# Kernel optimization log

Hardware: AMD Instinct MI355X
Metric: run time of the kernel (lower is better)

Reference implementation:

```python
import math
import jax, jax.numpy as jnp
import numpy as np

B, L, H, D = 1, 2048, 16, 64
M = 24            # nb_features
WINDOW = 128      # local_context / window_size
SCALE = 0.125     # softmax_scale = 1/sqrt(D)
MASK_VAL = -10000.0
EPS = 1e-4        # SBPerformerFeatures eps


def setup_inputs() -> dict:
    key = jax.random.key(0)
    k1, k2 = jax.random.split(key)
    qkv = jax.random.normal(k1, (B, L, 3, H, D), dtype=jnp.float32)
    proj = jax.random.normal(k2, (M, D), dtype=jnp.float32)  # Performer random features
    return {"qkv": qkv, "proj": proj}


def _performer_features(x, proj, is_query):
    # Softmax-kernel random features with separate log scale (scatterbrain SBPerformerFeatures).
    # exp(t*q.k) ~= exp(q_log + k_log) * <q_prime, k_prime>
    dn = math.sqrt(SCALE)
    xs = x * dn                                            # (b,h,l,d)
    x_dash = jnp.einsum('bhld,md->bhlm', xs, proj)         # (b,h,l,m)
    x_norm = 0.5 * jnp.sum(xs * xs, axis=-1, keepdims=True)
    half_log_m = 0.5 * math.log(M)
    if is_query:
        stab = jax.lax.stop_gradient(jnp.max(x_dash, axis=-1, keepdims=True))
        prime = jnp.exp(x_dash - stab) + EPS               # per-row stabilized
        log_scale = stab - x_norm - half_log_m             # (b,h,l,1)
    else:
        stab = jax.lax.stop_gradient(jnp.max(x_dash, axis=(-1, -2), keepdims=True))
        prime = jnp.exp(x_dash - x_norm - stab) + EPS      # norm folded in (needed for cumsum)
        log_scale = stab - half_log_m                      # (b,h,1,1)
    return prime, log_scale


def _band_mask(n):
    idx = jnp.arange(n)
    diff = idx[:, None] - idx[None, :]                     # i - j
    return jnp.where((diff >= 0) & (diff <= WINDOW), 0.0, MASK_VAL)  # (L,L)


def _forward(qkv, proj):
    q, k, v = qkv[:, :, 0], qkv[:, :, 1], qkv[:, :, 2]     # (b,l,h,d)
    q = jnp.transpose(q, (0, 2, 1, 3))                     # (b,h,l,d)
    k = jnp.transpose(k, (0, 2, 1, 3))
    v = jnp.transpose(v, (0, 2, 1, 3))

    # --- GlobalPerformer path ---
    q_prime, q_log = _performer_features(q, proj, True)    # (b,h,l,m), (b,h,l,1)
    k_prime, k_log = _performer_features(k, proj, False)   # (b,h,l,m), (b,h,1,1)
    global_scale = q_log + k_log                           # (b,h,l,1)

    k_cum = jnp.cumsum(k_prime, axis=2)
    global_out_cumsum = jnp.einsum('bhlm,bhlm->bhl', q_prime, k_cum)
    # causal_dot_product: out_i = q'_i . sum_{j<=i} k'_j v_j^T
    kv = jnp.cumsum(k_prime[..., :, None] * v[..., None, :], axis=2)   # (b,h,l,m,d)
    global_out = jnp.einsum('bhlm,bhlmd->bhld', q_prime, kv)

    mask = _band_mask(L)
    p_scores = jnp.einsum('bhme,bhne->bhmn', q_prime, k_prime) * SCALE
    global_qk = jnp.maximum(p_scores + mask[None, None], 0.0)  # masked_fill(<=0, 0)

    # --- Local exact softmax path ---
    scores = jnp.einsum('bhme,bhne->bhmn', q, k) * SCALE
    local_qk = scores + mask[None, None]
    qk_lse = jax.scipy.special.logsumexp(local_qk, axis=-1, keepdims=True)  # (b,h,l,1)

    gqk_sum = jnp.sum(global_qk, axis=-1, keepdims=True)
    global_log_norm = jnp.log(jnp.maximum(global_out_cumsum[..., None] - gqk_sum, 1e-24)) + global_scale
    log_norm = jnp.logaddexp(qk_lse, global_log_norm)      # (b,h,l,1)
    global_prime_scale = jnp.exp(global_scale - log_norm)  # (b,h,l,1)

    local_score = jax.nn.softmax(local_qk - log_norm, axis=-1) - global_qk * global_prime_scale
    out = jnp.einsum('bhmn,bhnd->bhmd', local_score, v) + global_out * global_prime_scale
    return jnp.transpose(out, (0, 2, 1, 3))                # (b,l,h,d)


def reference(qkv, proj):
    return _forward(qkv, proj)
```

## Files before the change

kernel.cpp:

```cpp
#include <hip/hip_runtime.h>
#include <hip/hip_bf16.h>

#define L_SEQ 2048
#define NH 16
#define DH 64
#define NCH 32
#define SCALE_F 0.125f
#define EPS_F 1e-4f
#define DN_F 0.35355339059327373f
#define HLM_F 1.5890269151739727f

typedef __attribute__((ext_vector_type(8))) short short8v;
typedef __attribute__((ext_vector_type(4))) float f32x4;

__device__ __forceinline__ unsigned short f2bf(float x) {
  unsigned u = __float_as_uint(x);
  u += 0x7FFFu + ((u >> 16) & 1u);
  return (unsigned short)(u >> 16);
}
__device__ __forceinline__ unsigned pk2(float a, float b) {
  return (unsigned)f2bf(a) | ((unsigned)f2bf(b) << 16);
}
__device__ __forceinline__ float stab_from_pmax(const float* __restrict__ pmax, int h, int t) {
  float v = pmax[h * 32 + (t & 31)];
  v = fmaxf(v, __shfl_xor(v, 1));  v = fmaxf(v, __shfl_xor(v, 2));
  v = fmaxf(v, __shfl_xor(v, 4));  v = fmaxf(v, __shfl_xor(v, 8));
  v = fmaxf(v, __shfl_xor(v, 16));
  return v;
}

__global__ __launch_bounds__(256) void k1_feat(
    const float* __restrict__ qkv, const float* __restrict__ proj,
    float* __restrict__ kdash, float* __restrict__ knorm,
    float* __restrict__ qdash, float* __restrict__ qnorm,
    float* __restrict__ pmax, unsigned* __restrict__ kbw, unsigned* __restrict__ qbw)
{
  __shared__ __attribute__((aligned(16))) float sP[24][68];
  __shared__ __attribute__((aligned(16))) float sX[64][68];
  __shared__ float sRed[256];
  const int c = blockIdx.x, h = blockIdx.y, qk = blockIdx.z, t = threadIdx.x;
  const int slot = qk ? 0 : 1;
  for (int i = t; i < 24 * 64; i += 256) sP[i >> 6][i & 63] = proj[i];
  for (int i = t; i < 1024; i += 256) {
    int rr = i >> 4, d4 = (i & 15) * 4;
    int l = c * 64 + rr;
    *(float4*)&sX[rr][d4] = *(const float4*)(qkv + (((size_t)l * 3 + slot) * NH + h) * DH + d4);
  }
  __syncthreads();
  unsigned* dstw = qk ? qbw : kbw;
  for (int w = t; w < 2048; w += 256) {
    int rr = w >> 5, wo = w & 31;
    int l = c * 64 + rr;
    float2 xv = *(const float2*)&sX[rr][2 * wo];
    dstw[((size_t)h * L_SEQ + l) * 32 + (wo ^ ((rr & 7) << 2))] = pk2(xv.x, xv.y);
  }
  const int r = t >> 2, mg = t & 3;
  float acc[6] = {0.f, 0.f, 0.f, 0.f, 0.f, 0.f};
  float sq = 0.f;
  for (int d4 = 0; d4 < 16; ++d4) {
    float4 xv = *(const float4*)&sX[r][d4 * 4];
    sq += xv.x * xv.x; sq += xv.y * xv.y; sq += xv.z * xv.z; sq += xv.w * xv.w;
#pragma unroll
    for (int i = 0; i < 6; ++i) {
      float4 pv = *(const float4*)&sP[mg * 6 + i][d4 * 4];
      acc[i] += xv.x * pv.x; acc[i] += xv.y * pv.y;
      acc[i] += xv.z * pv.z; acc[i] += xv.w * pv.w;
    }
  }
  int l = c * 64 + r;
  float* dsh = qk ? qdash : kdash;
  float lmax = -1e30f;
#pragma unroll
  for (int i = 0; i < 6; ++i) {
    float v = acc[i] * DN_F;
    dsh[((size_t)h * L_SEQ + l) * 24 + mg * 6 + i] = v;
    lmax = fmaxf(lmax, v);
  }
  if (mg == 0) (qk ? qnorm : knorm)[h * L_SEQ + l] = 0.5f * SCALE_F * sq;
  if (qk == 0) {
    sRed[t] = lmax;
    __syncthreads();
#pragma unroll
    for (int s = 128; s > 0; s >>= 1) {
      if (t < s) sRed[t] = fmaxf(sRed[t], sRed[t + s]);
      __syncthreads();
    }
    if (t == 0) pmax[h * 32 + c] = sRed[0];
  }
}

__global__ __launch_bounds__(256) void k3_kprime(
    const float* __restrict__ qkv, const float* __restrict__ kdash,
    const float* __restrict__ knorm, const float* __restrict__ pmax,
    unsigned* __restrict__ kpw, float* __restrict__ kpfx, float* __restrict__ kvs,
    unsigned* __restrict__ vtw)
{
  __shared__ float sKp[64][25];
  __shared__ __attribute__((aligned(16))) float sV[64][68];
  const int c = blockIdx.x, h = blockIdx.y, t = threadIdx.x;
  const float stab = stab_from_pmax(pmax, h, t);
  for (int i = t; i < 1024; i += 256) {
    int rr = i >> 4, d4 = (i & 15) * 4;
    int l = c * 64 + rr;
    *(float4*)&sV[rr][d4] = *(const float4*)(qkv + (((size_t)l * 3 + 2) * NH + h) * DH + d4);
  }
  for (int i = t; i < 1536; i += 256) {
    int r = i / 24, m = i % 24;
    int l = c * 64 + r;
    sKp[r][m] = __expf(kdash[((size_t)h * L_SEQ + l) * 24 + m] - knorm[h * L_SEQ + l] - stab) + EPS_F;
  }
  __syncthreads();
  for (int w = t; w < 1024; w += 256) {
    int r = w >> 4, wo = w & 15;
    int l = c * 64 + r;
    float a = (wo < 12) ? sKp[r][2 * wo] : 0.f;
    float bb = (wo < 12) ? sKp[r][2 * wo + 1] : 0.f;
    kpw[((size_t)h * L_SEQ + l) * 16 + (wo ^ ((r & 3) << 2))] = pk2(a, bb);
  }
  for (int w = t; w < 2048; w += 256) {
    int d = w >> 5, jp = w & 31;
    vtw[((size_t)h * NCH + c) * 2048 + d * 32 + (jp ^ ((d & 7) << 2))] = pk2(sV[2 * jp][d], sV[2 * jp + 1][d]);
  }
  if (t < 192) {
    const int m = t % 24, dO = (t / 24) * 8;
    float a0x = 0.f, a0y = 0.f, a0z = 0.f, a0w = 0.f;
    float a1x = 0.f, a1y = 0.f, a1z = 0.f, a1w = 0.f;
    for (int r2 = 0; r2 < 64; ++r2) {
      float kp = sKp[r2][m];
      float4 v0 = *(const float4*)&sV[r2][dO];
      float4 v1 = *(const float4*)&sV[r2][dO + 4];
      a0x += kp * v0.x; a0y += kp * v0.y; a0z += kp * v0.z; a0w += kp * v0.w;
      a1x += kp * v1.x; a1y += kp * v1.y; a1z += kp * v1.z; a1w += kp * v1.w;
    }
    float* dst = kvs + ((size_t)h * NCH + c) * 1536 + m * 64 + dO;
    float4 o0 = {a0x, a0y, a0z, a0w};
    float4 o1 = {a1x, a1y, a1z, a1w};
    *(float4*)dst = o0;
    *(float4*)(dst + 4) = o1;
  }
  if (t < 24) {
    float run = 0.f;
    for (int r2 = 0; r2 < 64; ++r2) {
      run += sKp[r2][t];
      kpfx[((size_t)h * L_SEQ + c * 64 + r2) * 24 + t] = run;
    }
  }
}

__global__ __launch_bounds__(256, 2) void k6_attn(
    const unsigned* __restrict__ kpw, const float* __restrict__ kpfx,
    const float* __restrict__ kvs, const unsigned* __restrict__ vtw,
    const float* __restrict__ qdash, const float* __restrict__ qnorm,
    const float* __restrict__ pmax, const unsigned* __restrict__ kbw,
    const unsigned* __restrict__ qbw, float* __restrict__ out)
{
  __shared__ __attribute__((aligned(16))) char lds[56160];
  char* sKW = lds;
  char* sKp = lds + 24576;
  char* sQV = lds + 36864;
  char* sQp = lds + 45056;
  float* sSum = (float*)(lds + 49152);
  float* sGps = sSum + 64;
  float* sRin = sGps + 64;
  float* sKcx = (float*)(lds + 49920);
  float* sPfx = (float*)(lds + 50016);

  const int b = blockIdx.x, h = blockIdx.y, t = threadIdx.x;
  const int wv = t >> 6, lane = t & 63, g = lane >> 4, ln = lane & 15;
  const int keybase = b * 64 - 128;
  const int jmin = (b >= 2) ? 0 : (128 - 64 * b);
  const int rA = wv * 16 + ln;

  for (int w = t; w < 1536; w += 256) {
    int r = w >> 3, q4 = w & 7;
    int l = keybase + r; l = l < 0 ? 0 : l;
    *(uint4*)(sKW + r * 128 + q4 * 16) = *(const uint4*)(kbw + ((size_t)h * L_SEQ + l) * 32 + q4 * 4);
  }
  for (int w = t; w < 512; w += 256) {
    int r = w >> 3, q4 = w & 7;
    int l = b * 64 + r;
    *(uint4*)(sQV + r * 128 + q4 * 16) = *(const uint4*)(qbw + ((size_t)h * L_SEQ + l) * 32 + q4 * 4);
  }
  for (int w = t; w < 768; w += 256) {
    int r = w >> 2, q4 = w & 3;
    int l = keybase + r; l = l < 0 ? 0 : l;
    *(uint4*)(sKp + r * 64 + q4 * 16) = *(const uint4*)(kpw + ((size_t)h * L_SEQ + l) * 16 + q4 * 4);
  }
  const float stab = stab_from_pmax(pmax, h, t);
  {
    float accp[6] = {0.f, 0.f, 0.f, 0.f, 0.f, 0.f};
    const float* srcb = kvs + (size_t)h * NCH * 1536 + t;
    int bp = 0;
    for (; bp + 4 <= b; bp += 4) {
      float v0[6], v1[6], v2[6], v3[6];
#pragma unroll
      for (int j = 0; j < 6; ++j) v0[j] = srcb[(size_t)(bp + 0) * 1536 + j * 256];
#pragma unroll
      for (int j = 0; j < 6; ++j) v1[j] = srcb[(size_t)(bp + 1) * 1536 + j * 256];
#pragma unroll
      for (int j = 0; j < 6; ++j) v2[j] = srcb[(size_t)(bp + 2) * 1536 + j * 256];
#pragma unroll
      for (int j = 0; j < 6; ++j) v3[j] = srcb[(size_t)(bp + 3) * 1536 + j * 256];
#pragma unroll
      for (int j = 0; j < 6; ++j) {
        accp[j] += v0[j]; accp[j] += v1[j]; accp[j] += v2[j]; accp[j] += v3[j];
      }
    }
    for (; bp < b; ++bp) {
#pragma unroll
      for (int j = 0; j < 6; ++j) accp[j] += srcb[(size_t)bp * 1536 + j * 256];
    }
#pragma unroll
    for (int j = 0; j < 6; ++j) sPfx[t + j * 256] = accp[j];
  }
  if (t < 24) {
    float runk = 0.f;
    for (int bp = 0; bp < b; ++bp)
      runk += kpfx[((size_t)h * L_SEQ + bp * 64 + 63) * 24 + t];
    sKcx[t] = runk;
  }
  float qlog = 0.f;
  float qpv[24];
  if (t < 64) {
    int r = t, l = b * 64 + r;
    const float* qdp = qdash + ((size_t)h * L_SEQ + l) * 24;
    float qd[24], mx = -1e30f;
#pragma unroll
    for (int m = 0; m < 24; ++m) { qd[m] = qdp[m]; mx = fmaxf(mx, qd[m]); }
#pragma unroll
    for (int m = 0; m < 24; ++m) qpv[m] = __expf(qd[m] - mx) + EPS_F;
    qlog = mx - qnorm[h * L_SEQ + l] - HLM_F;
#pragma unroll
    for (int wo = 0; wo < 16; ++wo) {
      float a = (wo < 12) ? qpv[2 * wo] : 0.f;
      float bb = (wo < 12) ? qpv[2 * wo + 1] : 0.f;
      *(unsigned*)(sQp + (r * 64 + (((wo * 4)) ^ ((r & 3) << 4)))) = pk2(a, bb);
    }
  }
  __syncthreads();

  float eF[12][4];
  float rs[4] = {0.f, 0.f, 0.f, 0.f};
  short8v aS0 = *(const short8v*)(sQV + (rA * 128 + ((g * 16) ^ ((rA & 7) << 4))));
  short8v aS1 = *(const short8v*)(sQV + (rA * 128 + ((64 + g * 16) ^ ((rA & 7) << 4))));
#pragma unroll
  for (int nt = 0; nt < 12; ++nt) {
    int rB = nt * 16 + ln;
    short8v b0 = *(const short8v*)(sKW + (rB * 128 + ((g * 16) ^ ((rB & 7) << 4))));
    short8v b1 = *(const short8v*)(sKW + (rB * 128 + ((64 + g * 16) ^ ((rB & 7) << 4))));
    f32x4 acc = {0.f, 0.f, 0.f, 0.f};
    acc = __builtin_amdgcn_mfma_f32_16x16x32_bf16(aS0, b0, acc, 0, 0, 0);
    acc = __builtin_amdgcn_mfma_f32_16x16x32_bf16(aS1, b1, acc, 0, 0, 0);
    int j = nt * 16 + ln;
#pragma unroll
    for (int reg = 0; reg < 4; ++reg) {
      int rl = wv * 16 + g * 4 + reg;
      float e = 0.f;
      if (j >= rl && j <= rl + 128 && j >= jmin) e = __expf(SCALE_F * acc[reg]);
      eF[nt][reg] = e;
      rs[reg] += e;
    }
  }
#pragma unroll
  for (int reg = 0; reg < 4; ++reg) {
    float v = rs[reg];
    v += __shfl_xor(v, 1); v += __shfl_xor(v, 2);
    v += __shfl_xor(v, 4); v += __shfl_xor(v, 8);
    if (ln == 0) sSum[wv * 16 + g * 4 + reg] = v;
  }

  float pF[12][4];
  short8v aP = *(const short8v*)(sQp + (rA * 64 + ((g * 16) ^ ((rA & 3) << 4))));
#pragma unroll
  for (int nt = 0; nt < 12; ++nt) {
    int rB = nt * 16 + ln;
    short8v bp = *(const short8v*)(sKp + (rB * 64 + ((g * 16) ^ ((rB & 3) << 4))));
    f32x4 acc = {0.f, 0.f, 0.f, 0.f};
    acc = __builtin_amdgcn_mfma_f32_16x16x32_bf16(aP, bp, acc, 0, 0, 0);
#pragma unroll
    for (int reg = 0; reg < 4; ++reg) pF[nt][reg] = acc[reg];
  }
  __syncthreads();

  if (t < 64) {
    int r = t, l = b * 64 + r;
    const float* kfc = kpfx + ((size_t)h * L_SEQ + l) * 24;
    int b1i = (b >= 1) ? b - 1 : 0;
    int b2i = (b >= 2) ? b - 2 : 0;
    int rm1 = (r >= 1) ? r - 1 : 0;
    const float* T1p = kpfx + ((size_t)h * L_SEQ + b1i * 64 + 63) * 24;
    const float* T2p = kpfx + ((size_t)h * L_SEQ + b2i * 64 + 63) * 24;
    const float* S2p = kpfx + ((size_t)h * L_SEQ + b2i * 64 + rm1) * 24;
    float f1 = (b >= 1) ? 1.f : 0.f;
    float f2 = (b >= 2) ? 1.f : 0.f;
    float fr = (b >= 2 && r >= 1) ? 1.f : 0.f;
    float psc = 0.f, kcs = 0.f, bnd = 0.f;
#pragma unroll
    for (int m = 0; m < 24; ++m) {
      float qp = qpv[m];
      float kc = kfc[m];
      psc += qp * kc;
      kcs += qp * sKcx[m];
      bnd += qp * (kc + f1 * T1p[m] + f2 * T2p[m] - fr * S2p[m]);
    }
    float goc = kcs + psc;
    float gqk = SCALE_F * bnd;
    float se = sSum[r];
    float lse = __logf(se);
    float gscale = qlog + stab - HLM_F;
    float gln = __logf(fmaxf(goc - gqk, 1e-24f)) + gscale;
    float mx2 = fmaxf(lse, gln), mn2 = fminf(lse, gln);
    float lognorm = mx2 + log1pf(__expf(mn2 - mx2));
    sGps[r] = __expf(gscale - lognorm);
    sRin[r] = 1.f / se;
  }
  __syncthreads();

  float gpr[4], rin[4];
#pragma unroll
  for (int reg = 0; reg < 4; ++reg) {
    int rl = wv * 16 + g * 4 + reg;
    gpr[reg] = sGps[rl];
    rin[reg] = sRin[rl];
  }
#pragma unroll
  for (int nt = 0; nt < 12; ++nt) {
    int j = nt * 16 + ln;
#pragma unroll
    for (int reg = 0; reg < 4; ++reg) {
      int rl = wv * 16 + g * 4 + reg;
      bool causal = (j >= 128) && (j <= 128 + rl);
      bool bprev = (j >= rl) && (j < 128) && (j >= jmin);
      float coef = causal ? (1.f - SCALE_F) * gpr[reg] : (bprev ? -SCALE_F * gpr[reg] : 0.f);
      float wgt = eF[nt][reg] * rin[reg] + coef * pF[nt][reg];
      float wn = __shfl_xor(wgt, 1);
      if ((ln & 1) == 0) {
        *(unsigned*)(sKW + (rl * 384 + ((j * 2) ^ ((rl & 7) << 4)))) = pk2(wgt, wn);
      }
    }
  }
  __syncthreads();

  for (int w = t; w < 1024; w += 256) {
    int d = w >> 4, mp = w & 15;
    int m0 = 2 * mp, m1 = m0 + 1;
    float a = (m0 < 24) ? sPfx[m0 * 64 + d] : 0.f;
    float bb = (m1 < 24) ? sPfx[m1 * 64 + d] : 0.f;
    *(unsigned*)(sKp + (d * 64 + ((mp * 4) ^ ((d & 3) << 4)))) = pk2(a, bb);
  }

  f32x4 oF[4];
#pragma unroll
  for (int dt = 0; dt < 4; ++dt) { f32x4 z = {0.f, 0.f, 0.f, 0.f}; oF[dt] = z; }
  for (int vt3 = 0; vt3 < 3; ++vt3) {
    int lt = b - 2 + vt3; lt = lt < 0 ? 0 : lt;
    for (int w = t; w < 512; w += 256) {
      *(uint4*)(sQV + w * 16) = *(const uint4*)(vtw + ((size_t)h * NCH + lt) * 2048 + w * 4);
    }
    __syncthreads();
#pragma unroll
    for (int ks = 0; ks < 2; ++ks) {
      short8v aw = *(const short8v*)(sKW + (rA * 384 + ((vt3 * 128 + ks * 64 + g * 16) ^ ((rA & 7) << 4))));
#pragma unroll
      for (int dt = 0; dt < 4; ++dt) {
        int rB = dt * 16 + ln;
        short8v bv = *(const short8v*)(sQV + (rB * 128 + ((ks * 64 + g * 16) ^ ((rB & 7) << 4))));
        oF[dt] = __builtin_amdgcn_mfma_f32_16x16x32_bf16(aw, bv, oF[dt], 0, 0, 0);
      }
    }
    __syncthreads();
  }

  short8v aq = *(const short8v*)(sQp + (rA * 64 + ((g * 16) ^ ((rA & 3) << 4))));
  f32x4 ogF[4];
#pragma unroll
  for (int dt = 0; dt < 4; ++dt) {
    int rB = dt * 16 + ln;
    short8v bg = *(const short8v*)(sKp + (rB * 64 + ((g * 16) ^ ((rB & 3) << 4))));
    f32x4 z = {0.f, 0.f, 0.f, 0.f};
    ogF[dt] = __builtin_amdgcn_mfma_f32_16x16x32_bf16(aq, bg, z, 0, 0, 0);
  }

#pragma unroll
  for (int dt = 0; dt < 4; ++dt) {
    int d = dt * 16 + ln;
#pragma unroll
    for (int reg = 0; reg < 4; ++reg) {
      int rl = wv * 16 + g * 4 + reg;
      int l = b * 64 + rl;
      out[((size_t)l * NH + h) * DH + d] = oF[dt][reg] + gpr[reg] * ogF[dt][reg];
    }
  }
}

extern "C" void kernel_launch(void* const* d_in, const int* in_sizes, int n_in,
                              void* d_out, int out_size, void* d_ws, size_t ws_size,
                              hipStream_t stream)
{
  const float* qkv = (const float*)d_in[0];
  const float* proj = (const float*)d_in[1];
  float* out = (float*)d_out;
  char* ws = (char*)d_ws;

  float* kdash   = (float*)(ws + 0);
  float* qdash   = (float*)(ws + 3145728);
  float* knorm   = (float*)(ws + 6291456);
  float* qnorm   = (float*)(ws + 6422528);
  float* pmax    = (float*)(ws + 6553600);
  unsigned* kbw  = (unsigned*)(ws + 6555648);
  unsigned* qbw  = (unsigned*)(ws + 10749952);
  unsigned* kpw  = (unsigned*)(ws + 14944256);
  float* kpfx    = (float*)(ws + 17041408);
  unsigned* vtw  = (unsigned*)(ws + 20187136);
  float* kvs     = (float*)(ws + 24381440);

  k1_feat<<<dim3(NCH, NH, 2), 256, 0, stream>>>(qkv, proj, kdash, knorm, qdash, qnorm, pmax, kbw, qbw);
  k3_kprime<<<dim3(NCH, NH), 256, 0, stream>>>(qkv, kdash, knorm, pmax, kpw, kpfx, kvs, vtw);
  k6_attn<<<dim3(NCH, NH), 256, 0, stream>>>(kpw, kpfx, kvs, vtw, qdash, qnorm, pmax, kbw, qbw, out);
}
```

Measured before the change: 120.6 us.

## Preload all V tiles into LDS upfront and drop per-tile barriers

All three V tiles used by the PV product are loaded into a larger LDS region during the prologue, alongside the other loads. This removes the per-tile global loads and the synchronisation barriers inside the PV loop. The k-prime prefix scan in the chunk kernel is moved to otherwise idle threads so it overlaps the kv accumulation, and qdash reads are vectorised. LDS per block grows substantially, which may reduce how many blocks fit per CU.

```diff
diff --git a/kernel.cpp b/kernel.cpp
--- a/kernel.cpp
+++ b/kernel.cpp
@@ -137,12 +137,12 @@
     float4 o1 = {a1x, a1y, a1z, a1w};
     *(float4*)dst = o0;
     *(float4*)(dst + 4) = o1;
-  }
-  if (t < 24) {
+  } else if (t < 216) {
+    const int m = t - 192;
     float run = 0.f;
     for (int r2 = 0; r2 < 64; ++r2) {
-      run += sKp[r2][t];
-      kpfx[((size_t)h * L_SEQ + c * 64 + r2) * 24 + t] = run;
+      run += sKp[r2][m];
+      kpfx[((size_t)h * L_SEQ + c * 64 + r2) * 24 + m] = run;
     }
   }
 }
@@ -154,16 +154,17 @@
     const float* __restrict__ pmax, const unsigned* __restrict__ kbw,
     const unsigned* __restrict__ qbw, float* __restrict__ out)
 {
-  __shared__ __attribute__((aligned(16))) char lds[56160];
+  __shared__ __attribute__((aligned(16))) char lds[80736];
   char* sKW = lds;
   char* sKp = lds + 24576;
-  char* sQV = lds + 36864;
-  char* sQp = lds + 45056;
-  float* sSum = (float*)(lds + 49152);
+  char* sV  = lds + 36864;
+  char* sQ  = lds + 61440;
+  char* sQp = lds + 69632;
+  float* sSum = (float*)(lds + 73728);
   float* sGps = sSum + 64;
   float* sRin = sGps + 64;
-  float* sKcx = (float*)(lds + 49920);
-  float* sPfx = (float*)(lds + 50016);
+  float* sKcx = (float*)(lds + 74496);
+  float* sPfx = (float*)(lds + 74592);
 
   const int b = blockIdx.x, h = blockIdx.y, t = threadIdx.x;
   const int wv = t >> 6, lane = t & 63, g = lane >> 4, ln = lane & 15;
@@ -179,12 +180,17 @@
   for (int w = t; w < 512; w += 256) {
     int r = w >> 3, q4 = w & 7;
     int l = b * 64 + r;
-    *(uint4*)(sQV + r * 128 + q4 * 16) = *(const uint4*)(qbw + ((size_t)h * L_SEQ + l) * 32 + q4 * 4);
+    *(uint4*)(sQ + r * 128 + q4 * 16) = *(const uint4*)(qbw + ((size_t)h * L_SEQ + l) * 32 + q4 * 4);
   }
   for (int w = t; w < 768; w += 256) {
     int r = w >> 2, q4 = w & 3;
     int l = keybase + r; l = l < 0 ? 0 : l;
     *(uint4*)(sKp + r * 64 + q4 * 16) = *(const uint4*)(kpw + ((size_t)h * L_SEQ + l) * 16 + q4 * 4);
+  }
+  for (int w = t; w < 1536; w += 256) {
+    int vt = w >> 9, idx = w & 511;
+    int lt = b - 2 + vt; lt = lt < 0 ? 0 : lt;
+    *(uint4*)(sV + vt * 8192 + idx * 16) = *(const uint4*)(vtw + ((size_t)h * NCH + lt) * 2048 + idx * 4);
   }
   const float stab = stab_from_pmax(pmax, h, t);
   {
@@ -224,9 +230,15 @@
   if (t < 64) {
     int r = t, l = b * 64 + r;
     const float* qdp = qdash + ((size_t)h * L_SEQ + l) * 24;
-    float qd[24], mx = -1e30f;
-#pragma unroll
-    for (int m = 0; m < 24; ++m) { qd[m] = qdp[m]; mx = fmaxf(mx, qd[m]); }
+    float qd[24];
+#pragma unroll
+    for (int i = 0; i < 6; ++i) {
+      float4 v = *(const float4*)(qdp + 4 * i);
+      qd[4 * i] = v.x; qd[4 * i + 1] = v.y; qd[4 * i + 2] = v.z; qd[4 * i + 3] = v.w;
+    }
+    float mx = -1e30f;
+#pragma unroll
+    for (int m = 0; m < 24; ++m) mx = fmaxf(mx, qd[m]);
 #pragma unroll
     for (int m = 0; m < 24; ++m) qpv[m] = __expf(qd[m] - mx) + EPS_F;
     qlog = mx - qnorm[h * L_SEQ + l] - HLM_F;
@@ -241,8 +253,8 @@
 
   float eF[12][4];
   float rs[4] = {0.f, 0.f, 0.f, 0.f};
-  short8v aS0 = *(const short8v*)(sQV + (rA * 128 + ((g * 16) ^ ((rA & 7) << 4))));
-  short8v aS1 = *(const short8v*)(sQV + (rA * 128 + ((64 + g * 16) ^ ((rA & 7) << 4))));
+  short8v aS0 = *(const short8v*)(sQ + (rA * 128 + ((g * 16) ^ ((rA & 7) << 4))));
+  short8v aS1 = *(const short8v*)(sQ + (rA * 128 + ((64 + g * 16) ^ ((rA & 7) << 4))));
 #pragma unroll
   for (int nt = 0; nt < 12; ++nt) {
     int rB = nt * 16 + ln;
@@ -352,24 +364,21 @@
   f32x4 oF[4];
 #pragma unroll
   for (int dt = 0; dt < 4; ++dt) { f32x4 z = {0.f, 0.f, 0.f, 0.f}; oF[dt] = z; }
+#pragma unroll
   for (int vt3 = 0; vt3 < 3; ++vt3) {
-    int lt = b - 2 + vt3; lt = lt < 0 ? 0 : lt;
-    for (int w = t; w < 512; w += 256) {
-      *(uint4*)(sQV + w * 16) = *(const uint4*)(vtw + ((size_t)h * NCH + lt) * 2048 + w * 4);
-    }
-    __syncthreads();
+    const char* vbase = sV + vt3 * 8192;
 #pragma unroll
     for (int ks = 0; ks < 2; ++ks) {
       short8v aw = *(const short8v*)(sKW + (rA * 384 + ((vt3 * 128 + ks * 64 + g * 16) ^ ((rA & 7) << 4))));
 #pragma unroll
       for (int dt = 0; dt < 4; ++dt) {
         int rB = dt * 16 + ln;
-        short8v bv = *(const short8v*)(sQV + (rB * 128 + ((ks * 64 + g * 16) ^ ((rB & 7) << 4))));
+        short8v bv = *(const short8v*)(vbase + (rB * 128 + ((ks * 64 + g * 16) ^ ((rB & 7) << 4))));
         oF[dt] = __builtin_amdgcn_mfma_f32_16x16x32_bf16(aw, bv, oF[dt], 0, 0, 0);
       }
     }
-    __syncthreads();
-  }
+  }
+  __syncthreads();
 
   short8v aq = *(const short8v*)(sQp + (rA * 64 + ((g * 16) ^ ((rA & 3) << 4))));
   f32x4 ogF[4];
```

After: 120.0 us. About the same (-0.5%).
